# Optimization experiments

Hardware: AMD Instinct MI355X
Metric: run time of the kernel (lower is better)

## Reference

```python
import jax, jax.numpy as jnp
import numpy as np

N_NODES = 100000
N_EDGES = 1600000
HID = 256
HEADS = 4
HEAD_DIM = HID // HEADS
EPS = 1e-5


def _layernorm(x, g, b):
    mu = jnp.mean(x, axis=-1, keepdims=True)
    var = jnp.mean(jnp.square(x - mu), axis=-1, keepdims=True)
    return (x - mu) * jax.lax.rsqrt(var + EPS) * g + b


def setup_inputs() -> dict:
    key = jax.random.key(0)
    ks = jax.random.split(key, 16)
    s = 0.05  # small init, mimics xavier gain=0.1
    inp = {
        'h': jax.random.normal(ks[0], (N_NODES, HID), jnp.float32),
        'src': jax.random.randint(ks[1], (N_EDGES,), 0, N_NODES, jnp.int32),
        'dst': jax.random.randint(ks[2], (N_EDGES,), 0, N_NODES, jnp.int32),
        'Wq': jax.random.normal(ks[3], (HID, HID), jnp.float32) * s,
        'bq': jnp.zeros((HID,), jnp.float32),
        'Wk': jax.random.normal(ks[4], (HID, HID), jnp.float32) * s,
        'bk': jnp.zeros((HID,), jnp.float32),
        'Wv': jax.random.normal(ks[5], (HID, HID), jnp.float32) * s,
        'bv': jnp.zeros((HID,), jnp.float32),
        'Wo': jax.random.normal(ks[6], (HID, HID), jnp.float32) * s,
        'bo': jnp.zeros((HID,), jnp.float32),
        'W1': jax.random.normal(ks[7], (HID, 2 * HID), jnp.float32) * s,
        'b1': jnp.zeros((2 * HID,), jnp.float32),
        'W2': jax.random.normal(ks[8], (2 * HID, HID), jnp.float32) * s,
        'b2': jnp.zeros((HID,), jnp.float32),
        'g1': jnp.ones((HID,), jnp.float32),
        'be1': jnp.zeros((HID,), jnp.float32),
        'g2': jnp.ones((HID,), jnp.float32),
        'be2': jnp.zeros((HID,), jnp.float32),
    }
    return inp


def reference(h, src, dst, Wq, bq, Wk, bk, Wv, bv, Wo, bo, W1, b1, W2, b2, g1, be1, g2, be2):
    N = h.shape[0]
    scale = HEAD_DIM ** -0.5
    h_norm = _layernorm(h, g1, be1)
    Q = (h_norm @ Wq + bq).reshape(N, HEADS, HEAD_DIM)
    K = (h_norm @ Wk + bk).reshape(N, HEADS, HEAD_DIM)
    V = (h_norm @ Wv + bv).reshape(N, HEADS, HEAD_DIM)

    # per-edge attention logits: q from dst, k from src  -> [E, heads]
    logits = jnp.einsum('ehd,ehd->eh', Q[dst], K[src]) * scale

    # edge softmax grouped by destination node (dgl.ops.edge_softmax)
    seg_max = jax.ops.segment_max(logits, dst, num_segments=N)  # [N, heads]
    e = jnp.exp(logits - seg_max[dst])
    seg_sum = jax.ops.segment_sum(e, dst, num_segments=N)
    w = e / seg_sum[dst]  # [E, heads]

    # message = V[src] * attn ; aggregate by sum over incoming edges
    msg = V[src] * w[:, :, None]  # [E, heads, head_dim]
    h_new = jax.ops.segment_sum(msg, dst, num_segments=N).reshape(N, HID)

    h_attn = h_new @ Wo + bo
    h = h + h_attn  # dropout is identity in eval
    h2 = _layernorm(h, g2, be2)
    ffn = jax.nn.relu(h2 @ W1 + b1) @ W2 + b2
    return h + ffn
```

## Files before the change

### kernel.cpp

```cpp
#include <hip/hip_runtime.h>
#include <hip/hip_bf16.h>

#define NN 100000
#define NE 1600000

typedef __attribute__((ext_vector_type(8))) short bf16x8;
typedef __attribute__((ext_vector_type(4))) float f32x4;
typedef __attribute__((ext_vector_type(2))) float f32x2;
typedef __attribute__((ext_vector_type(2))) unsigned int u32x2;
typedef __attribute__((ext_vector_type(4))) unsigned int u32x4;

__device__ __forceinline__ float bf2f(unsigned short u) {
    union { unsigned int i; float f; } c; c.i = ((unsigned int)u) << 16; return c.f;
}
__device__ __forceinline__ unsigned short f2bf(float f) {
    union { float f; unsigned int i; } c; c.f = f;
    unsigned int lsb = (c.i >> 16) & 1u;
    c.i += 0x7FFFu + lsb;
    return (unsigned short)(c.i >> 16);
}
__device__ __forceinline__ u32x4 pack8bf(f32x4 a, f32x4 b) {
    u32x4 p;
    p.x = f2bf(a[0]) | ((unsigned int)f2bf(a[1]) << 16);
    p.y = f2bf(a[2]) | ((unsigned int)f2bf(a[3]) << 16);
    p.z = f2bf(b[0]) | ((unsigned int)f2bf(b[1]) << 16);
    p.w = f2bf(b[2]) | ((unsigned int)f2bf(b[3]) << 16);
    return p;
}
__device__ __forceinline__ unsigned int pack4fp8(f32x4 v) {
    unsigned int w = __builtin_amdgcn_cvt_pk_fp8_f32(v[0], v[1], 0, false);
    return __builtin_amdgcn_cvt_pk_fp8_f32(v[2], v[3], w, true);
}
__device__ __forceinline__ void gload_lds16(const void* g, void* l) {
    __builtin_amdgcn_global_load_lds(
        (const __attribute__((address_space(1))) void*)g,
        (__attribute__((address_space(3))) void*)l, 16, 0, 0);
}

__global__ __launch_bounds__(256) void ln_k(
    const float* __restrict__ x, const float* __restrict__ g,
    const float* __restrict__ b, unsigned short* __restrict__ y, int nrows)
{
    int w = threadIdx.x >> 6, lane = threadIdx.x & 63;
    int row = blockIdx.x * 4 + w;
    if (row >= nrows) return;
    const float4 xv = *(const float4*)(x + (size_t)row * 256 + lane * 4);
    float s  = xv.x + xv.y + xv.z + xv.w;
    float sq = xv.x*xv.x + xv.y*xv.y + xv.z*xv.z + xv.w*xv.w;
    #pragma unroll
    for (int m = 1; m < 64; m <<= 1) {
        s  += __shfl_xor(s,  m);
        sq += __shfl_xor(sq, m);
    }
    float mu  = s * (1.0f / 256.0f);
    float var = sq * (1.0f / 256.0f) - mu * mu;
    float r = rsqrtf(var + 1e-5f);
    float4 gv = *(const float4*)(g + lane * 4);
    float4 bv = *(const float4*)(b + lane * 4);
    ushort4 o;
    o.x = f2bf((xv.x - mu) * r * gv.x + bv.x);
    o.y = f2bf((xv.y - mu) * r * gv.y + bv.y);
    o.z = f2bf((xv.z - mu) * r * gv.z + bv.z);
    o.w = f2bf((xv.w - mu) * r * gv.w + bv.w);
    *(ushort4*)(y + (size_t)row * 256 + lane * 4) = o;
}

__global__ __launch_bounds__(256) void wcv_all_k(
    const float* __restrict__ Wq, const float* __restrict__ Wk, const float* __restrict__ Wv,
    const float* __restrict__ Wo, const float* __restrict__ W1, const float* __restrict__ W2,
    unsigned short* __restrict__ Wqkvt, unsigned short* __restrict__ Wot,
    unsigned short* __restrict__ W1t, unsigned short* __restrict__ W2t,
    const float* __restrict__ bq, const float* __restrict__ bk, const float* __restrict__ bv,
    float* __restrict__ bqkv)
{
    int id = blockIdx.x;
    int t = threadIdx.x;
    if (id == 512) {
        bqkv[t] = bq[t]; bqkv[256 + t] = bk[t]; bqkv[512 + t] = bv[t];
        return;
    }
    const float* W; unsigned short* Wt; int K, N, kx, ny;
    if (id < 192) {
        int grp = id >> 6, l = id & 63;
        W = (grp == 0) ? Wq : ((grp == 1) ? Wk : Wv);
        Wt = Wqkvt + grp * 256 * 256;
        K = 256; N = 256; kx = l & 7; ny = l >> 3;
    } else if (id < 256) {
        int l = id - 192; W = Wo; Wt = Wot; K = 256; N = 256; kx = l & 7; ny = l >> 3;
    } else if (id < 384) {
        int l = id - 256; W = W1; Wt = W1t; K = 256; N = 512; kx = l & 7; ny = l >> 3;
    } else {
        int l = id - 384; W = W2; Wt = W2t; K = 512; N = 256; kx = l & 15; ny = l >> 4;
    }
    __shared__ unsigned short tl[32][33];
    int bk2 = kx * 32, bn = ny * 32;
    int lx = t & 31, ly = t >> 5;
    #pragma unroll
    for (int r = 0; r < 32; r += 8)
        tl[ly + r][lx] = f2bf(W[(size_t)(bk2 + ly + r) * N + bn + lx]);
    __syncthreads();
    #pragma unroll
    for (int r = 0; r < 32; r += 8)
        Wt[(size_t)(bn + ly + r) * K + bk2 + lx] = tl[lx][ly + r];
}

template<int NBX, int OMODE, bool RELU, bool RES>
__global__ __launch_bounds__(512) void mgemm_k(
    const unsigned short* __restrict__ A, const unsigned short* __restrict__ Wt,
    const float* __restrict__ bias, void* __restrict__ outv, void* __restrict__ out2,
    const void* __restrict__ res, const float* __restrict__ g, const float* __restrict__ be,
    int M, int N, int K)
{
    __shared__ __align__(16) char lds[49152];
    const int t = threadIdx.x;
    const int lane = t & 63;
    const int wid = t >> 6;
    const int wm = wid >> 2, wn = wid & 3;

    int bmi, bni;
    if (NBX > 0) {
        const int nwg = gridDim.x;
        const int q = nwg >> 3, r = nwg & 7;
        const int xcd = blockIdx.x & 7, idx = blockIdx.x >> 3;
        const int wgid = (xcd < r) ? (xcd * (q + 1) + idx)
                                   : (r * (q + 1) + (xcd - r) * q + idx);
        bmi = wgid / NBX; bni = wgid - bmi * NBX;
    } else {
        bmi = blockIdx.y; bni = blockIdx.x;
    }
    const int bm = bmi * 128, bn = bni * 256;

    f32x4 acc[4][4] = {};

    const int ra_s = t >> 2;
    const int sa_s = (t & 3) ^ (ra_s & 3);
    const size_t arow = (size_t)min(bm + ra_s, M - 1) * K + sa_s * 8;
    const int rb0 = t >> 2;
    const int sb0 = (t & 3) ^ (rb0 & 3);
    const int rb1 = (512 + t) >> 2;
    const int sb1 = (t & 3) ^ (rb1 & 3);
    const size_t brow0 = (size_t)(bn + rb0) * K + sb0 * 8;
    const size_t brow1 = (size_t)(bn + rb1) * K + sb1 * 8;

    const int fr = lane & 15, fs = lane >> 4;
    const int rslot = fs ^ (fr & 3);

    const int KS = K >> 5;
    int cur = 0;
    {
        unsigned short* Ab = (unsigned short*)(lds);
        unsigned short* Bb = (unsigned short*)(lds + 16384);
        gload_lds16(A + arow, Ab + t * 8);
        gload_lds16(Wt + brow0, Bb + t * 8);
        gload_lds16(Wt + brow1, Bb + (512 + t) * 8);
    }
    for (int ks = 0; ks < KS; ++ks) {
        __syncthreads();
        if (ks + 1 < KS) {
            int k1 = (ks + 1) << 5;
            unsigned short* Ab = (unsigned short*)(lds + (cur ^ 1) * 8192);
            unsigned short* Bb = (unsigned short*)(lds + 16384 + (cur ^ 1) * 16384);
            gload_lds16(A + arow + k1, Ab + t * 8);
            gload_lds16(Wt + brow0 + k1, Bb + t * 8);
            gload_lds16(Wt + brow1 + k1, Bb + (512 + t) * 8);
        }
        const unsigned short* As = (const unsigned short*)(lds + cur * 8192);
        const unsigned short* Bs = (const unsigned short*)(lds + 16384 + cur * 16384);
        bf16x8 af[4], bf[4];
        #pragma unroll
        for (int fm = 0; fm < 4; ++fm)
            af[fm] = *(const bf16x8*)&As[(wm * 64 + fm * 16 + fr) * 32 + rslot * 8];
        #pragma unroll
        for (int fn = 0; fn < 4; ++fn)
            bf[fn] = *(const bf16x8*)&Bs[(wn * 64 + fn * 16 + fr) * 32 + rslot * 8];
        #pragma unroll
        for (int fm = 0; fm < 4; ++fm)
            #pragma unroll
            for (int fn = 0; fn < 4; ++fn)
                acc[fm][fn] = __builtin_amdgcn_mfma_f32_16x16x32_bf16(
                    af[fm], bf[fn], acc[fm][fn], 0, 0, 0);
        cur ^= 1;
    }
    __syncthreads();

    float* wl = (float*)(lds + wid * 4352);
    float* stats = (float*)(lds + 34816);
    const int rr = lane >> 2;
    const int c4 = (lane & 3) * 16;
    const int qg = lane >> 4;

    #pragma unroll
    for (int fm = 0; fm < 4; ++fm) {
        #pragma unroll
        for (int fn = 0; fn < 4; ++fn)
            #pragma unroll
            for (int i = 0; i < 4; ++i)
                wl[(qg * 4 + i) * 68 + fn * 16 + fr] = acc[fm][fn][i];
        f32x4 v0 = *(const f32x4*)&wl[rr * 68 + c4 + 0];
        f32x4 v1 = *(const f32x4*)&wl[rr * 68 + c4 + 4];
        f32x4 v2 = *(const f32x4*)&wl[rr * 68 + c4 + 8];
        f32x4 v3 = *(const f32x4*)&wl[rr * 68 + c4 + 12];
        const int rowg = bm + wm * 64 + fm * 16 + rr;
        const int colg = bn + wn * 64 + c4;
        if (rowg < M) {
            v0 += *(const f32x4*)&bias[colg + 0];
            v1 += *(const f32x4*)&bias[colg + 4];
            v2 += *(const f32x4*)&bias[colg + 8];
            v3 += *(const f32x4*)&bias[colg + 12];
            if (RES) {
                if (OMODE == 4) {
                    const unsigned short* rp = (const unsigned short*)res + (size_t)rowg * N + colg;
                    u32x4 ra = *(const u32x4*)rp;
                    u32x4 rb = *(const u32x4*)(rp + 8);
                    v0[0] += bf2f(ra.x & 0xffff); v0[1] += bf2f(ra.x >> 16);
                    v0[2] += bf2f(ra.y & 0xffff); v0[3] += bf2f(ra.y >> 16);
                    v1[0] += bf2f(ra.z & 0xffff); v1[1] += bf2f(ra.z >> 16);
                    v1[2] += bf2f(ra.w & 0xffff); v1[3] += bf2f(ra.w >> 16);
                    v2[0] += bf2f(rb.x & 0xffff); v2[1] += bf2f(rb.x >> 16);
                    v2[2] += bf2f(rb.y & 0xffff); v2[3] += bf2f(rb.y >> 16);
                    v3[0] += bf2f(rb.z & 0xffff); v3[1] += bf2f(rb.z >> 16);
                    v3[2] += bf2f(rb.w & 0xffff); v3[3] += bf2f(rb.w >> 16);
                } else {
                    const float* rp = (const float*)res + (size_t)rowg * N + colg;
                    v0 += *(const f32x4*)(rp + 0);
                    v1 += *(const f32x4*)(rp + 4);
                    v2 += *(const f32x4*)(rp + 8);
                    v3 += *(const f32x4*)(rp + 12);
                }
            }
            if (RELU) {
                #pragma unroll
                for (int j = 0; j < 4; ++j) {
                    v0[j] = fmaxf(v0[j], 0.f); v1[j] = fmaxf(v1[j], 0.f);
                    v2[j] = fmaxf(v2[j], 0.f); v3[j] = fmaxf(v3[j], 0.f);
                }
            }
        } else {
            v0 = 0.f; v1 = 0.f; v2 = 0.f; v3 = 0.f;
        }

        if (OMODE == 3) {
            acc[fm][0] = v0; acc[fm][1] = v1; acc[fm][2] = v2; acc[fm][3] = v3;
        } else if (rowg < M) {
            if (OMODE == 0 || OMODE == 4) {
                float* op = (float*)outv + (size_t)rowg * N + colg;
                *(f32x4*)(op + 0) = v0; *(f32x4*)(op + 4) = v1;
                *(f32x4*)(op + 8) = v2; *(f32x4*)(op + 12) = v3;
            } else if (OMODE == 1) {
                unsigned short* op = (unsigned short*)outv + (size_t)rowg * N + colg;
                *(u32x4*)(op + 0) = pack8bf(v0, v1);
                *(u32x4*)(op + 8) = pack8bf(v2, v3);
            } else {
                if (colg < 256) {
                    unsigned short* op = (unsigned short*)outv + (size_t)rowg * 256 + colg;
                    *(u32x4*)(op + 0) = pack8bf(v0, v1);
                    *(u32x4*)(op + 8) = pack8bf(v2, v3);
                } else {
                    u32x4 p8;
                    p8.x = pack4fp8(v0); p8.y = pack4fp8(v1);
                    p8.z = pack4fp8(v2); p8.w = pack4fp8(v3);
                    *(u32x4*)((unsigned char*)out2 + (size_t)rowg * 512 + (colg - 256)) = p8;
                }
            }
        }
    }

    if (OMODE == 3) {
        #pragma unroll
        for (int fm = 0; fm < 4; ++fm) {
            float s = 0.f, q = 0.f;
            #pragma unroll
            for (int j = 0; j < 4; ++j)
                #pragma unroll
                for (int c = 0; c < 4; ++c) {
                    float x = acc[fm][j][c];
                    s += x; q += x * x;
                }
            s += __shfl_xor(s, 1); q += __shfl_xor(q, 1);
            s += __shfl_xor(s, 2); q += __shfl_xor(q, 2);
            if ((lane & 3) == 0) {
                int rowl = wm * 64 + fm * 16 + rr;
                stats[rowl * 8 + wn * 2 + 0] = s;
                stats[rowl * 8 + wn * 2 + 1] = q;
            }
        }
        __syncthreads();
        #pragma unroll
        for (int fm = 0; fm < 4; ++fm) {
            const int rowl = wm * 64 + fm * 16 + rr;
            const int rowg = bm + rowl;
            float s = stats[rowl * 8 + 0] + stats[rowl * 8 + 2] + stats[rowl * 8 + 4] + stats[rowl * 8 + 6];
            float q = stats[rowl * 8 + 1] + stats[rowl * 8 + 3] + stats[rowl * 8 + 5] + stats[rowl * 8 + 7];
            float mu = s * (1.0f / 256.0f);
            float var = q * (1.0f / 256.0f) - mu * mu;
            float rstd = rsqrtf(var + 1e-5f);
            const int colg = bn + wn * 64 + c4;
            if (rowg < M) {
                unsigned short* mp = (unsigned short*)out2 + (size_t)rowg * 256 + colg;
                *(u32x4*)(mp + 0) = pack8bf(acc[fm][0], acc[fm][1]);
                *(u32x4*)(mp + 8) = pack8bf(acc[fm][2], acc[fm][3]);
                f32x4 nv[4];
                #pragma unroll
                for (int j = 0; j < 4; ++j) {
                    f32x4 gv = *(const f32x4*)&g[colg + j * 4];
                    f32x4 bv = *(const f32x4*)&be[colg + j * 4];
                    #pragma unroll
                    for (int c = 0; c < 4; ++c)
                        nv[j][c] = (acc[fm][j][c] - mu) * rstd * gv[c] + bv[c];
                }
                unsigned short* op = (unsigned short*)outv + (size_t)rowg * 256 + colg;
                *(u32x4*)(op + 0) = pack8bf(nv[0], nv[1]);
                *(u32x4*)(op + 8) = pack8bf(nv[2], nv[3]);
            }
        }
    }
}

__global__ void degcnt_k(const int* __restrict__ dst, int* __restrict__ deg, int E)
{
    int e = blockIdx.x * blockDim.x + threadIdx.x;
    if (e < E) atomicAdd(deg + dst[e], 1);
}

__global__ __launch_bounds__(1024) void scanA_k(int* __restrict__ a, int* __restrict__ aux, int n)
{
    __shared__ int wsum[16];
    __shared__ int wpre[16];
    int t = threadIdx.x, lane = t & 63, w = t >> 6;
    int i = blockIdx.x * 1024 + t;
    int v = (i < n) ? a[i] : 0;
    int s = v;
    #pragma unroll
    for (int d = 1; d < 64; d <<= 1) {
        int u = __shfl_up(s, d);
        if (lane >= d) s += u;
    }
    if (lane == 63) wsum[w] = s;
    __syncthreads();
    if (t == 0) {
        int run = 0;
        #pragma unroll
        for (int j = 0; j < 16; ++j) { wpre[j] = run; run += wsum[j]; }
        aux[blockIdx.x] = run;
    }
    __syncthreads();
    if (i < n) a[i] = wpre[w] + s - v;
}

__global__ __launch_bounds__(128) void scanB_k(int* __restrict__ aux, int* __restrict__ tot, int nb)
{
    __shared__ int ws[2];
    int t = threadIdx.x, lane = t & 63, w = t >> 6;
    int v = (t < nb) ? aux[t] : 0;
    int s = v;
    #pragma unroll
    for (int d = 1; d < 64; d <<= 1) {
        int u = __shfl_up(s, d);
        if (lane >= d) s += u;
    }
    if (lane == 63) ws[w] = s;
    __syncthreads();
    int add = (w == 1) ? ws[0] : 0;
    if (t < nb) aux[t] = add + s - v;
    if (t == nb - 1) tot[0] = add + s;
}

__global__ __launch_bounds__(1024) void scanC_k(int* __restrict__ a, const int* __restrict__ aux, int n)
{
    int i = blockIdx.x * 1024 + threadIdx.x;
    if (i < n) a[i] += aux[blockIdx.x];
}

__global__ void scatter_k(
    const int* __restrict__ dst, const int* __restrict__ srcarr,
    const int* __restrict__ off, int* __restrict__ cursor,
    int* __restrict__ csr, int E)
{
    int e = blockIdx.x * blockDim.x + threadIdx.x;
    if (e >= E) return;
    int d = dst[e];
    int pos = off[d] + atomicAdd(cursor + d, 1);
    csr[pos] = srcarr[e];
}

__global__ __launch_bounds__(256) void attn_k(
    const int* __restrict__ csr, const int* __restrict__ off,
    const unsigned short* __restrict__ Q, const unsigned char* __restrict__ KV8,
    unsigned short* __restrict__ hnew)
{
    int w = threadIdx.x >> 6, lane = threadIdx.x & 63;
    int n = blockIdx.x * 4 + w;
    if (n >= NN) return;
    int e0 = off[n], e1 = off[n + 1];

    u32x2 qr = __builtin_nontemporal_load((const u32x2*)(Q + (size_t)n * 256 + lane * 4));
    const float q0 = bf2f((unsigned short)(qr.x & 0xffff)) * 0.125f;
    const float q1 = bf2f((unsigned short)(qr.x >> 16))    * 0.125f;
    const float q2 = bf2f((unsigned short)(qr.y & 0xffff)) * 0.125f;
    const float q3 = bf2f((unsigned short)(qr.y >> 16))    * 0.125f;

    float s = 0.f;
    float a0 = 0.f, a1 = 0.f, a2 = 0.f, a3 = 0.f;

    int i = e0;
    for (; i + 7 < e1; i += 8) {
        int ns[8];
        #pragma unroll
        for (int j = 0; j < 8; ++j) ns[j] = csr[i + j];
        unsigned int kd[8], vd[8];
        #pragma unroll
        for (int j = 0; j < 8; ++j) {
            const unsigned char* r = KV8 + (size_t)ns[j] * 512 + lane * 4;
            kd[j] = *(const unsigned int*)r;
            vd[j] = *(const unsigned int*)(r + 256);
        }
        float l[8];
        #pragma unroll
        for (int j = 0; j < 8; ++j) {
            f32x2 ka = __builtin_amdgcn_cvt_pk_f32_fp8(kd[j], false);
            f32x2 kb = __builtin_amdgcn_cvt_pk_f32_fp8(kd[j], true);
            l[j] = q0 * ka.x + q1 * ka.y + q2 * kb.x + q3 * kb.y;
        }
        #pragma unroll
        for (int m2 = 1; m2 < 16; m2 <<= 1) {
            #pragma unroll
            for (int j = 0; j < 8; ++j) l[j] += __shfl_xor(l[j], m2);
        }
        #pragma unroll
        for (int j = 0; j < 8; ++j) {
            float p = __expf(l[j]);
            f32x2 va = __builtin_amdgcn_cvt_pk_f32_fp8(vd[j], false);
            f32x2 vb = __builtin_amdgcn_cvt_pk_f32_fp8(vd[j], true);
            s  += p;
            a0 += p * va.x; a1 += p * va.y;
            a2 += p * vb.x; a3 += p * vb.y;
        }
    }
    for (; i + 3 < e1; i += 4) {
        int ns[4];
        #pragma unroll
        for (int j = 0; j < 4; ++j) ns[j] = csr[i + j];
        unsigned int kd[4], vd[4];
        #pragma unroll
        for (int j = 0; j < 4; ++j) {
            const unsigned char* r = KV8 + (size_t)ns[j] * 512 + lane * 4;
            kd[j] = *(const unsigned int*)r;
            vd[j] = *(const unsigned int*)(r + 256);
        }
        float l[4];
        #pragma unroll
        for (int j = 0; j < 4; ++j) {
            f32x2 ka = __builtin_amdgcn_cvt_pk_f32_fp8(kd[j], false);
            f32x2 kb = __builtin_amdgcn_cvt_pk_f32_fp8(kd[j], true);
            l[j] = q0 * ka.x + q1 * ka.y + q2 * kb.x + q3 * kb.y;
        }
        #pragma unroll
        for (int m2 = 1; m2 < 16; m2 <<= 1) {
            #pragma unroll
            for (int j = 0; j < 4; ++j) l[j] += __shfl_xor(l[j], m2);
        }
        #pragma unroll
        for (int j = 0; j < 4; ++j) {
            float p = __expf(l[j]);
            f32x2 va = __builtin_amdgcn_cvt_pk_f32_fp8(vd[j], false);
            f32x2 vb = __builtin_amdgcn_cvt_pk_f32_fp8(vd[j], true);
            s  += p;
            a0 += p * va.x; a1 += p * va.y;
            a2 += p * vb.x; a3 += p * vb.y;
        }
    }
    for (; i < e1; ++i) {
        int n0 = csr[i];
        const unsigned char* r = KV8 + (size_t)n0 * 512 + lane * 4;
        unsigned int kd = *(const unsigned int*)r;
        unsigned int vd = *(const unsigned int*)(r + 256);
        f32x2 ka = __builtin_amdgcn_cvt_pk_f32_fp8(kd, false);
        f32x2 kb = __builtin_amdgcn_cvt_pk_f32_fp8(kd, true);
        float l0 = q0 * ka.x + q1 * ka.y + q2 * kb.x + q3 * kb.y;
        #pragma unroll
        for (int m2 = 1; m2 < 16; m2 <<= 1) l0 += __shfl_xor(l0, m2);
        float p = __expf(l0);
        f32x2 va = __builtin_amdgcn_cvt_pk_f32_fp8(vd, false);
        f32x2 vb = __builtin_amdgcn_cvt_pk_f32_fp8(vd, true);
        s  += p;
        a0 += p * va.x; a1 += p * va.y;
        a2 += p * vb.x; a3 += p * vb.y;
    }
    float inv = (e1 > e0) ? 1.0f / s : 0.f;
    u32x2 ov;
    ov.x = ((unsigned int)f2bf(a1 * inv) << 16) | f2bf(a0 * inv);
    ov.y = ((unsigned int)f2bf(a3 * inv) << 16) | f2bf(a2 * inv);
    __builtin_nontemporal_store(ov, (u32x2*)(hnew + (size_t)n * 256 + lane * 4));
}

extern "C" void kernel_launch(void* const* d_in, const int* in_sizes, int n_in,
                              void* d_out, int out_size, void* d_ws, size_t ws_size,
                              hipStream_t stream)
{
    if (n_in < 19) return;
    const float* h   = (const float*)d_in[0];
    const int*   src = (const int*)d_in[1];
    const int*   dst = (const int*)d_in[2];
    const float* Wq  = (const float*)d_in[3];
    const float* bq  = (const float*)d_in[4];
    const float* Wk  = (const float*)d_in[5];
    const float* bk  = (const float*)d_in[6];
    const float* Wv  = (const float*)d_in[7];
    const float* bv  = (const float*)d_in[8];
    const float* Wo  = (const float*)d_in[9];
    const float* bo  = (const float*)d_in[10];
    const float* W1  = (const float*)d_in[11];
    const float* b1  = (const float*)d_in[12];
    const float* W2  = (const float*)d_in[13];
    const float* b2  = (const float*)d_in[14];
    const float* g1  = (const float*)d_in[15];
    const float* be1 = (const float*)d_in[16];
    const float* g2  = (const float*)d_in[17];
    const float* be2 = (const float*)d_in[18];
    float* out = (float*)d_out;

    char* w = (char*)d_ws;
    unsigned short* hnormb = (unsigned short*)(w + 0);
    unsigned short* Qb     = (unsigned short*)(w + 51200000);
    unsigned char*  KV8    = (unsigned char*)(w + 102400000);
    int*            degoff = (int*)(w + 153600000);
    int*            cursor = (int*)(w + 154000384);
    int*            csr    = (int*)(w + 154400768);
    unsigned short* Wqkvt  = (unsigned short*)(w + 204800000);
    unsigned short* Wot    = (unsigned short*)(w + 205193216);
    unsigned short* W1t    = (unsigned short*)(w + 205324288);
    unsigned short* W2t    = (unsigned short*)(w + 205586432);
    float*          bqkv   = (float*)(w + 205848576);
    int*            scanaux= (int*)(w + 205851648);
    unsigned short* hnewb  = hnormb;
    unsigned short* h2nb   = hnormb;
    unsigned short* hmidb  = Qb;
    unsigned short* ffnmid = (unsigned short*)(w + 102400000);

    hipMemsetAsync(degoff, 0, 400384, stream);
    hipMemsetAsync(cursor, 0, 400384, stream);

    const int M = NN;
    dim3 blk(256);
    dim3 blk512(512);
    const int MB = (M + 127) / 128;
    const int SCAN_BLKS = (NN + 1023) / 1024;

    wcv_all_k<<<dim3(513), blk, 0, stream>>>(Wq, Wk, Wv, Wo, W1, W2,
                                             Wqkvt, Wot, W1t, W2t, bq, bk, bv, bqkv);

    degcnt_k<<<dim3((NE + 255) / 256), blk, 0, stream>>>(dst, degoff, NE);
    scanA_k<<<dim3(SCAN_BLKS), dim3(1024), 0, stream>>>(degoff, scanaux, NN);
    scanB_k<<<dim3(1), dim3(128), 0, stream>>>(scanaux, degoff + NN, SCAN_BLKS);
    scanC_k<<<dim3(SCAN_BLKS), dim3(1024), 0, stream>>>(degoff, scanaux, NN);
    scatter_k<<<dim3((NE + 255) / 256), blk, 0, stream>>>(dst, src, degoff, cursor, csr, NE);

    ln_k<<<dim3((NN + 3) / 4), blk, 0, stream>>>(h, g1, be1, hnormb, NN);

    mgemm_k<3, 2, false, false><<<dim3(3 * MB), blk512, 0, stream>>>(
        hnormb, Wqkvt, bqkv, Qb, KV8, nullptr, nullptr, nullptr, M, 768, 256);

    attn_k<<<dim3((NN + 3) / 4), blk, 0, stream>>>(csr, degoff, Qb, KV8, hnewb);

    dim3 go(1, MB);
    mgemm_k<0, 3, false, true><<<go, blk512, 0, stream>>>(
        hnewb, Wot, bo, h2nb, hmidb, h, g2, be2, M, 256, 256);

    mgemm_k<2, 1, true, false><<<dim3(2 * MB), blk512, 0, stream>>>(
        h2nb, W1t, b1, ffnmid, nullptr, nullptr, nullptr, nullptr, M, 512, 256);
    mgemm_k<0, 4, false, true><<<go, blk512, 0, stream>>>(
        ffnmid, W2t, b2, out, nullptr, hmidb, nullptr, nullptr, M, 256, 512);
}
```

Measured before the change: 594.2 us.

## Triple-buffer GEMM LDS staging with explicit vmcnt waits

Moves the bf16 MFMA GEMM main loop from double to triple buffering in LDS. Loads are issued two K-steps ahead, and each step waits with s_waitcnt vmcnt on the older loads before a raw barrier, so global-to-LDS latency overlaps with more compute. LDS per block grows from 48KB to 72KB, which may reduce the number of resident workgroups. The hand-written waitcnt also assumes each stage issues exactly three loads.

```diff
diff --git a/kernel.cpp b/kernel.cpp
--- a/kernel.cpp
+++ b/kernel.cpp
@@ -111,7 +111,7 @@
     const void* __restrict__ res, const float* __restrict__ g, const float* __restrict__ be,
     int M, int N, int K)
 {
-    __shared__ __align__(16) char lds[49152];
+    __shared__ __align__(16) char lds[73728];
     const int t = threadIdx.x;
     const int lane = t & 63;
     const int wid = t >> 6;
@@ -146,26 +146,28 @@
     const int rslot = fs ^ (fr & 3);
 
     const int KS = K >> 5;
+
+#define STAGE(b, k0) { \
+        unsigned short* Ab = (unsigned short*)(lds + (b) * 8192); \
+        unsigned short* Bb = (unsigned short*)(lds + 24576 + (b) * 16384); \
+        const int kk_ = (k0) << 5; \
+        gload_lds16(A + arow + kk_, Ab + t * 8); \
+        gload_lds16(Wt + brow0 + kk_, Bb + t * 8); \
+        gload_lds16(Wt + brow1 + kk_, Bb + (512 + t) * 8); }
+
+    STAGE(0, 0)
+    STAGE(1, 1)
     int cur = 0;
-    {
-        unsigned short* Ab = (unsigned short*)(lds);
-        unsigned short* Bb = (unsigned short*)(lds + 16384);
-        gload_lds16(A + arow, Ab + t * 8);
-        gload_lds16(Wt + brow0, Bb + t * 8);
-        gload_lds16(Wt + brow1, Bb + (512 + t) * 8);
-    }
     for (int ks = 0; ks < KS; ++ks) {
-        __syncthreads();
-        if (ks + 1 < KS) {
-            int k1 = (ks + 1) << 5;
-            unsigned short* Ab = (unsigned short*)(lds + (cur ^ 1) * 8192);
-            unsigned short* Bb = (unsigned short*)(lds + 16384 + (cur ^ 1) * 16384);
-            gload_lds16(A + arow + k1, Ab + t * 8);
-            gload_lds16(Wt + brow0 + k1, Bb + t * 8);
-            gload_lds16(Wt + brow1 + k1, Bb + (512 + t) * 8);
+        if (ks + 1 < KS) asm volatile("s_waitcnt vmcnt(3)" ::: "memory");
+        else             asm volatile("s_waitcnt vmcnt(0)" ::: "memory");
+        __builtin_amdgcn_s_barrier();
+        if (ks + 2 < KS) {
+            int nb = cur + 2; if (nb >= 3) nb -= 3;
+            STAGE(nb, ks + 2)
         }
         const unsigned short* As = (const unsigned short*)(lds + cur * 8192);
-        const unsigned short* Bs = (const unsigned short*)(lds + 16384 + cur * 16384);
+        const unsigned short* Bs = (const unsigned short*)(lds + 24576 + cur * 16384);
         bf16x8 af[4], bf[4];
         #pragma unroll
         for (int fm = 0; fm < 4; ++fm)
@@ -179,8 +181,9 @@
             for (int fn = 0; fn < 4; ++fn)
                 acc[fm][fn] = __builtin_amdgcn_mfma_f32_16x16x32_bf16(
                     af[fm], bf[fn], acc[fm][fn], 0, 0, 0);
-        cur ^= 1;
-    }
+        if (++cur == 3) cur = 0;
+    }
+#undef STAGE
     __syncthreads();
 
     float* wl = (float*)(lds + wid * 4352);
```

Result: faster. 579.2 us (-2.5%).
